# Kernel tuning notes

Measured on AMD Instinct MI355X. Metric: run time of the kernel, lower is better.

## Reference

```python
import jax, jax.numpy as jnp
import numpy as np

N = 4096        # num_queries == gnn_query_dim
C1 = 1001       # classes + 1
D = 4096        # gnn_query_dim
H_MLP = 1024    # mlp_hidden_dim
H = 256         # hidden_dim
O = 256         # output_dim
TOP_K = 32
BN_EPS = 1e-5


def setup_inputs() -> dict:
    key = jax.random.key(0)
    ks = jax.random.split(key, 14)
    def lin(kw, fan_in, shape):
        s = 1.0 / np.sqrt(fan_in)
        return jax.random.uniform(kw, shape, jnp.float32, -s, s)
    return {
        "probs": jax.random.uniform(ks[0], (N, C1), jnp.float32),
        "bbox_coords": jax.random.uniform(ks[1], (N, 4), jnp.float32),
        "query_emb": jax.random.normal(ks[2], (N, D), jnp.float32) * 0.02,
        "node_emb": jax.random.normal(ks[3], (N, D), jnp.float32) * 0.02,
        "mlp_w1": lin(ks[4], D + 4 + C1, (D + 4 + C1, H_MLP)),
        "mlp_b1": lin(ks[5], D + 4 + C1, (H_MLP,)),
        "mlp_w2": lin(ks[6], H_MLP, (H_MLP, N)),
        "mlp_b2": lin(ks[7], H_MLP, (N,)),
        "conv_w1": lin(ks[8], D, (D, H)),
        "conv_b1": lin(ks[9], D, (H,)),
        "conv_w2": lin(ks[10], H, (H, O)),
        "conv_b2": lin(ks[11], H, (O,)),
        "bn_gamma": jnp.ones((H,), jnp.float32),
        "bn_beta": jnp.zeros((H,), jnp.float32),
    }


def reference(probs, bbox_coords, query_emb, node_emb,
              mlp_w1, mlp_b1, mlp_w2, mlp_b2,
              conv_w1, conv_b1, conv_w2, conv_b2,
              bn_gamma, bn_beta):
    # edge-weight MLP -> dense dynamic adjacency logits (N, N)
    ew_in = jnp.concatenate([query_emb, probs, bbox_coords], axis=-1)
    h = jax.nn.relu(ew_in @ mlp_w1 + mlp_b1)
    adj = h @ mlp_w2 + mlp_b2                      # (N, N)

    # top-k neighbors per node (sparse dynamic graph)
    vals, idx = jax.lax.top_k(adj, TOP_K)          # (N, K), (N, K)

    # GCN symmetric normalization from row-degree (sum of top-k weights)
    deg = jnp.sum(vals, axis=-1)                   # (N,)
    dinv = jnp.where(deg > 0, jax.lax.rsqrt(jnp.maximum(deg, 1e-12)), 0.0)
    wn = vals * dinv[:, None] * dinv[idx]          # (N, K)

    def gcn_conv(x, w, b):
        # gather neighbor features, weighted sum, then linear
        msg = jnp.einsum('nk,nkf->nf', wn, x[idx])  # (N, F)
        return msg @ w + b

    out = gcn_conv(node_emb, conv_w1, conv_b1)      # (N, H)
    # BatchNorm1d (batch statistics, training-mode math)
    mean = jnp.mean(out, axis=0)
    var = jnp.var(out, axis=0)
    out = (out - mean) * jax.lax.rsqrt(var + BN_EPS) * bn_gamma + bn_beta
    out = jax.nn.relu(out)
    # dropout is identity in eval mode
    out = gcn_conv(out, conv_w2, conv_b2)           # (N, O)
    return out
```

## Files before the change

### kernel.cpp

```cpp
#include <hip/hip_runtime.h>
#include <cfloat>

#define N_NODES 4096
#define C1_DIM  1001
#define D_DIM   4096
#define HMLP    1024
#define KCAT    (D_DIM + C1_DIM + 4)
#define K1PAD   5120
#define TOPK    32

typedef unsigned short u16;
typedef __bf16 bf16x8 __attribute__((ext_vector_type(8)));
typedef u16    u16x8  __attribute__((ext_vector_type(8)));
typedef float  f32x4  __attribute__((ext_vector_type(4)));

__device__ __forceinline__ u16 f2bf(float f) {
  unsigned u = __float_as_uint(f);
  u += 0x7FFFu + ((u >> 16) & 1u);
  return (u16)(u >> 16);
}
__device__ __forceinline__ float bf2f(u16 h) {
  return __uint_as_float(((unsigned)h) << 16);
}

__device__ __forceinline__ void gload16(const void* g, void* l) {
  __builtin_amdgcn_global_load_lds(
      (const __attribute__((address_space(1))) unsigned int*)g,
      (__attribute__((address_space(3))) unsigned int*)l, 16, 0, 0);
}

__global__ __launch_bounds__(256) void transpose_split(
    const float* __restrict__ in, int R, int C, int Rpad,
    u16* __restrict__ out_hi, u16* __restrict__ out_lo) {
  __shared__ float t[64][65];
  const int rb = blockIdx.x * 64;
  const int cb = blockIdx.y * 64;
  const int tid = threadIdx.x;
  const int lr = tid >> 6, lc = tid & 63;
#pragma unroll
  for (int i = 0; i < 16; ++i) {
    const int r = lr + i * 4;
    const int gr = rb + r;
    t[r][lc] = (gr < R) ? in[(size_t)gr * C + cb + lc] : 0.f;
  }
  __syncthreads();
#pragma unroll
  for (int i = 0; i < 16; ++i) {
    const int c = lr + i * 4;
    const float v = t[lc][c];
    const u16 hi = f2bf(v);
    const u16 lo = f2bf(v - bf2f(hi));
    const size_t o = (size_t)(cb + c) * Rpad + rb + lc;
    out_hi[o] = hi; out_lo[o] = lo;
  }
}

template<int AMODE, bool RELU, bool OUT_SPLIT, bool HASBIAS>
__device__ __forceinline__ void gemm_body(
    int bx, int by,
    const u16* __restrict__ Ahi, const u16* __restrict__ Alo,
    const float* __restrict__ Aq,
    const float* __restrict__ probs, const float* __restrict__ bbox,
    const u16* __restrict__ Bthi, const u16* __restrict__ Btlo,
    const float* __restrict__ bias,
    float* __restrict__ Cf, u16* __restrict__ Chi, u16* __restrict__ Clo,
    int N, int K, u16* lds) {
  const int tid = threadIdx.x;
  const int lane = tid & 63, wave = tid >> 6;
  const int row0 = by * 128, col0 = bx * 64;
  const int wr0 = (wave >> 1) * 64, wc0 = (wave & 1) * 32;
  const int srow = tid >> 2, skof = (tid & 3) * 8;
  const int wu = (tid & ~63) * 8;

  f32x4 acc[4][2];
#pragma unroll
  for (int mi = 0; mi < 4; ++mi)
#pragma unroll
    for (int ni = 0; ni < 2; ++ni) acc[mi][ni] = (f32x4){0.f, 0.f, 0.f, 0.f};

  auto stageB = [&](int buf, int k0) {
    u16* base = lds + buf * 12288;
    gload16(Bthi + (size_t)(col0 + srow) * K + k0 + skof, base + 8192 + wu);
    gload16(Btlo + (size_t)(col0 + srow) * K + k0 + skof, base + 10240 + wu);
  };
  auto stageA0 = [&](int buf, int k0) {
    u16* base = lds + buf * 12288;
    gload16(Ahi + (size_t)(row0 + srow) * K + k0 + skof,      base + wu);
    gload16(Ahi + (size_t)(row0 + 64 + srow) * K + k0 + skof, base + 2048 + wu);
    gload16(Alo + (size_t)(row0 + srow) * K + k0 + skof,      base + 4096 + wu);
    gload16(Alo + (size_t)(row0 + 64 + srow) * K + k0 + skof, base + 6144 + wu);
  };
  auto loadA1 = [&](int k0, float4* x) {
    const int kk = k0 + skof;
#pragma unroll
    for (int j = 0; j < 2; ++j) {
      const int grow = row0 + srow + j * 64;
      if (kk < D_DIM) {
        const float* src = Aq + (size_t)grow * D_DIM + kk;
        x[j * 2]     = *(const float4*)src;
        x[j * 2 + 1] = *(const float4*)(src + 4);
      } else {
        float v[8];
#pragma unroll
        for (int e = 0; e < 8; ++e) {
          const int c = kk + e - D_DIM;
          v[e] = (c < C1_DIM) ? probs[(size_t)grow * C1_DIM + c]
               : (c < C1_DIM + 4) ? bbox[(size_t)grow * 4 + (c - C1_DIM)] : 0.f;
        }
        x[j * 2]     = make_float4(v[0], v[1], v[2], v[3]);
        x[j * 2 + 1] = make_float4(v[4], v[5], v[6], v[7]);
      }
    }
  };
  auto writeA1 = [&](int buf, const float4* x) {
    u16* base = lds + buf * 12288;
#pragma unroll
    for (int j = 0; j < 2; ++j) {
      const float xs[8] = {x[j*2].x, x[j*2].y, x[j*2].z, x[j*2].w,
                           x[j*2+1].x, x[j*2+1].y, x[j*2+1].z, x[j*2+1].w};
      u16x8 hi, lo;
#pragma unroll
      for (int e = 0; e < 8; ++e) {
        const u16 hh = f2bf(xs[e]);
        hi[e] = hh;
        lo[e] = f2bf(xs[e] - bf2f(hh));
      }
      *(u16x8*)&base[(srow + j * 64) * 32 + skof] = hi;
      *(u16x8*)&base[4096 + (srow + j * 64) * 32 + skof] = lo;
    }
  };
  auto compute = [&](int buf) {
    u16* base = lds + buf * 12288;
    const int ko = (lane >> 4) * 8;
    const int ar = lane & 15;
    bf16x8 ah[4], al[4], bh[2], bl[2];
#pragma unroll
    for (int mi = 0; mi < 4; ++mi) {
      const int r = wr0 + mi * 16 + ar;
      ah[mi] = *(const bf16x8*)&base[r * 32 + ko];
      al[mi] = *(const bf16x8*)&base[4096 + r * 32 + ko];
    }
#pragma unroll
    for (int ni = 0; ni < 2; ++ni) {
      const int c = wc0 + ni * 16 + ar;
      bh[ni] = *(const bf16x8*)&base[8192 + c * 32 + ko];
      bl[ni] = *(const bf16x8*)&base[10240 + c * 32 + ko];
    }
#pragma unroll
    for (int mi = 0; mi < 4; ++mi)
#pragma unroll
      for (int ni = 0; ni < 2; ++ni) {
        acc[mi][ni] = __builtin_amdgcn_mfma_f32_16x16x32_bf16(ah[mi], bh[ni], acc[mi][ni], 0, 0, 0);
        acc[mi][ni] = __builtin_amdgcn_mfma_f32_16x16x32_bf16(ah[mi], bl[ni], acc[mi][ni], 0, 0, 0);
        acc[mi][ni] = __builtin_amdgcn_mfma_f32_16x16x32_bf16(al[mi], bh[ni], acc[mi][ni], 0, 0, 0);
      }
  };

  int cur = 0;
  if (AMODE == 0) {
    stageA0(0, 0); stageB(0, 0);
    __syncthreads();
    for (int k0 = 0; k0 < K; k0 += 32) {
      if (k0 + 32 < K) { stageA0(cur ^ 1, k0 + 32); stageB(cur ^ 1, k0 + 32); }
      compute(cur);
      __syncthreads();
      cur ^= 1;
    }
  } else {
    float4 x[4];
    loadA1(0, x); stageB(0, 0); writeA1(0, x);
    __syncthreads();
    for (int k0 = 0; k0 < K; k0 += 32) {
      const bool nx = (k0 + 32 < K);
      float4 xn[4];
      if (nx) { loadA1(k0 + 32, xn); stageB(cur ^ 1, k0 + 32); }
      compute(cur);
      if (nx) writeA1(cur ^ 1, xn);
      __syncthreads();
      cur ^= 1;
    }
  }

#pragma unroll
  for (int mi = 0; mi < 4; ++mi)
#pragma unroll
    for (int ni = 0; ni < 2; ++ni) {
      const int gcol = col0 + wc0 + ni * 16 + (lane & 15);
      const float b = HASBIAS ? bias[gcol] : 0.f;
#pragma unroll
      for (int r = 0; r < 4; ++r) {
        const int grow = row0 + wr0 + mi * 16 + (lane >> 4) * 4 + r;
        float v = acc[mi][ni][r] + b;
        if (RELU) v = fmaxf(v, 0.f);
        if (OUT_SPLIT) {
          const u16 hi = f2bf(v);
          Chi[(size_t)grow * N + gcol] = hi;
          Clo[(size_t)grow * N + gcol] = f2bf(v - bf2f(hi));
        } else {
          Cf[(size_t)grow * N + gcol] = v;
        }
      }
    }
}

__global__ __launch_bounds__(256, 2) void gemm1_kernel(
    const float* __restrict__ query, const float* __restrict__ probs,
    const float* __restrict__ bbox,
    const u16* __restrict__ w1t_hi, const u16* __restrict__ w1t_lo,
    const float* __restrict__ b1,
    u16* __restrict__ h_hi, u16* __restrict__ h_lo) {
  __shared__ u16 lds[2 * 12288];
  gemm_body<1, true, true, true>(blockIdx.x, blockIdx.y,
      nullptr, nullptr, query, probs, bbox, w1t_hi, w1t_lo, b1,
      nullptr, h_hi, h_lo, HMLP, K1PAD, lds);
}

__global__ __launch_bounds__(256, 2) void fused2_kernel(
    const u16* __restrict__ h_hi, const u16* __restrict__ h_lo,
    const u16* __restrict__ w2t_hi, const u16* __restrict__ w2t_lo,
    const float* __restrict__ b2, float* __restrict__ adj,
    const float* __restrict__ node,
    const u16* __restrict__ w1ct_hi, const u16* __restrict__ w1ct_lo,
    float* __restrict__ Z1) {
  __shared__ u16 lds[2 * 12288];
  const int bid = blockIdx.x;
  if (bid < 128) {
    gemm_body<1, false, false, false>(bid & 3, bid >> 2,
        nullptr, nullptr, node, nullptr, nullptr, w1ct_hi, w1ct_lo, nullptr,
        Z1, nullptr, nullptr, 256, D_DIM, lds);
  } else {
    const int r = bid - 128;
    gemm_body<0, false, false, true>(r & 63, r >> 6,
        h_hi, h_lo, nullptr, nullptr, nullptr, w2t_hi, w2t_lo, b2,
        adj, nullptr, nullptr, N_NODES, HMLP, lds);
  }
}

__global__ __launch_bounds__(256) void gemm_small(
    const float* __restrict__ A, const float* __restrict__ B,
    float* __restrict__ C, int M, int Ncols, int K) {
  __shared__ float As[16][68];
  __shared__ float Bs[16][68];
  const int tid = threadIdx.x;
  const int row0 = blockIdx.y * 64, col0 = blockIdx.x * 64;
  const int tx = tid & 15, ty = tid >> 4;
  const int arow = tid >> 2, acol = (tid & 3) * 4;
  const int brow = tid >> 4, bcol = (tid & 15) * 4;

  float acc[4][4];
#pragma unroll
  for (int i = 0; i < 4; ++i)
#pragma unroll
    for (int j = 0; j < 4; ++j) acc[i][j] = 0.f;

  for (int k0 = 0; k0 < K; k0 += 16) {
    const float4 a4 = *(const float4*)(A + (size_t)(row0 + arow) * K + k0 + acol);
    const float4 b4 = *(const float4*)(B + (size_t)(k0 + brow) * Ncols + col0 + bcol);
    __syncthreads();
    As[acol + 0][arow] = a4.x; As[acol + 1][arow] = a4.y;
    As[acol + 2][arow] = a4.z; As[acol + 3][arow] = a4.w;
    *(float4*)&Bs[brow][bcol] = b4;
    __syncthreads();
#pragma unroll
    for (int k = 0; k < 16; ++k) {
      float av[4], bw[4];
      *(float4*)&av[0] = *(const float4*)&As[k][ty * 4];
      *(float4*)&bw[0] = *(const float4*)&Bs[k][tx * 4];
#pragma unroll
      for (int i = 0; i < 4; ++i)
#pragma unroll
        for (int j = 0; j < 4; ++j) acc[i][j] += av[i] * bw[j];
    }
  }

#pragma unroll
  for (int i = 0; i < 4; ++i) {
    const int r = row0 + ty * 4 + i;
    float4 v;
    v.x = acc[i][0]; v.y = acc[i][1]; v.z = acc[i][2]; v.w = acc[i][3];
    *(float4*)(C + (size_t)r * Ncols + col0 + tx * 4) = v;
  }
}

__global__ __launch_bounds__(256) void topk_kernel(
    const float* __restrict__ adj, float* __restrict__ vals,
    int* __restrict__ idxo, float* __restrict__ dinv) {
  __shared__ float sv[N_NODES];
  __shared__ float rw[4];
  __shared__ int   iw[4];
  const int n = blockIdx.x, tid = threadIdx.x;
  const int lane = tid & 63, wave = tid >> 6;
  const float4* rowp = (const float4*)(adj + (size_t)n * N_NODES);

  float mv = -FLT_MAX; int mi = 0x7FFFFFFF;
  for (int g = tid; g < N_NODES / 4; g += 256) {
    const float4 v4 = rowp[g];
    *(float4*)&sv[g * 4] = v4;
    if (v4.x > mv) { mv = v4.x; mi = g * 4 + 0; }
    if (v4.y > mv) { mv = v4.y; mi = g * 4 + 1; }
    if (v4.z > mv) { mv = v4.z; mi = g * 4 + 2; }
    if (v4.w > mv) { mv = v4.w; mi = g * 4 + 3; }
  }

  float sum = 0.f;
  for (int it = 0; it < TOPK; ++it) {
    float bv = mv; int bi = mi;
#pragma unroll
    for (int off = 1; off < 64; off <<= 1) {
      const float ov = __shfl_xor(bv, off);
      const int   oi = __shfl_xor(bi, off);
      if (ov > bv || (ov == bv && oi < bi)) { bv = ov; bi = oi; }
    }
    if (lane == 0) { rw[wave] = bv; iw[wave] = bi; }
    __syncthreads();
    bv = rw[0]; bi = iw[0];
#pragma unroll
    for (int w = 1; w < 4; ++w) {
      const float ov = rw[w]; const int oi = iw[w];
      if (ov > bv || (ov == bv && oi < bi)) { bv = ov; bi = oi; }
    }
    if (tid == 0) {
      vals[(size_t)n * TOPK + it] = bv;
      idxo[(size_t)n * TOPK + it] = bi;
    }
    sum += bv;
    if (tid == ((bi >> 2) & 255)) {
      sv[bi] = -FLT_MAX;
      mv = -FLT_MAX; mi = 0x7FFFFFFF;
      for (int g = tid; g < N_NODES / 4; g += 256) {
#pragma unroll
        for (int e = 0; e < 4; ++e) {
          const float v = sv[g * 4 + e];
          if (v > mv) { mv = v; mi = g * 4 + e; }
        }
      }
    }
    __syncthreads();
  }
  if (tid == 0)
    dinv[n] = (sum > 0.f) ? rsqrtf(fmaxf(sum, 1e-12f)) : 0.f;
}

__global__ __launch_bounds__(256) void agg_kernel(
    const float* __restrict__ Z, const float* __restrict__ vals,
    const int* __restrict__ idxo, const float* __restrict__ dinv,
    const float* __restrict__ bias, float* __restrict__ out) {
  const int n = blockIdx.x, f = threadIdx.x;
  const float dn = dinv[n];
  float acc = bias[f];
#pragma unroll
  for (int k = 0; k < TOPK; ++k) {
    const int   j = idxo[n * TOPK + k];
    const float w = vals[n * TOPK + k] * dn * dinv[j];
    acc += w * Z[(size_t)j * 256 + f];
  }
  out[(size_t)n * 256 + f] = acc;
}

__global__ __launch_bounds__(256) void bn_partial(
    const float* __restrict__ x, float* __restrict__ partial) {
  const int b = blockIdx.x, c = threadIdx.x;
  float s = 0.f, s2 = 0.f;
  for (int r = b * 32; r < b * 32 + 32; ++r) {
    const float v = x[(size_t)r * 256 + c];
    s += v; s2 += v * v;
  }
  partial[(size_t)b * 512 + c]       = s;
  partial[(size_t)b * 512 + 256 + c] = s2;
}

__global__ __launch_bounds__(256) void bn_reduce(
    const float* __restrict__ partial, float* __restrict__ colstats) {
  const int j = blockIdx.x, t = threadIdx.x;
  __shared__ float red[128];
  if (t < 128) red[t] = partial[(size_t)t * 512 + j];
  __syncthreads();
  for (int s = 64; s > 0; s >>= 1) {
    if (t < s) red[t] += red[t + s];
    __syncthreads();
  }
  if (t == 0) colstats[j] = red[0];
}

__global__ __launch_bounds__(256) void bn_apply(
    float* __restrict__ x, const float* __restrict__ colstats,
    const float* __restrict__ gamma, const float* __restrict__ beta) {
  const int i = blockIdx.x * 256 + threadIdx.x;
  const int c = i & 255;
  const float mean = colstats[c] * (1.f / 4096.f);
  float var = colstats[256 + c] * (1.f / 4096.f) - mean * mean;
  var = fmaxf(var, 0.f);
  const float v = (x[i] - mean) * rsqrtf(var + 1e-5f) * gamma[c] + beta[c];
  x[i] = fmaxf(v, 0.f);
}

extern "C" void kernel_launch(void* const* d_in, const int* in_sizes, int n_in,
                              void* d_out, int out_size, void* d_ws, size_t ws_size,
                              hipStream_t stream) {
  const float* probs   = (const float*)d_in[0];
  const float* bbox    = (const float*)d_in[1];
  const float* query   = (const float*)d_in[2];
  const float* node    = (const float*)d_in[3];
  const float* mlp_w1  = (const float*)d_in[4];
  const float* mlp_b1  = (const float*)d_in[5];
  const float* mlp_w2  = (const float*)d_in[6];
  const float* mlp_b2  = (const float*)d_in[7];
  const float* conv_w1 = (const float*)d_in[8];
  const float* conv_b1 = (const float*)d_in[9];
  const float* conv_w2 = (const float*)d_in[10];
  const float* conv_b2 = (const float*)d_in[11];
  const float* gamma   = (const float*)d_in[12];
  const float* beta    = (const float*)d_in[13];

  float* ws = (float*)d_ws;
  size_t off = 0;
  float* adj  = ws + off;  off += (size_t)N_NODES * N_NODES;
  u16* w1t_hi = (u16*)(ws + off);
  u16* w1t_lo = w1t_hi + (size_t)HMLP * K1PAD;
  off += (size_t)HMLP * K1PAD;
  u16* h_hi = (u16*)(ws + off);
  u16* h_lo = h_hi + (size_t)N_NODES * HMLP;
  off += (size_t)N_NODES * HMLP;
  u16* w1ct_hi = (u16*)(ws + off);
  u16* w1ct_lo = w1ct_hi + (size_t)256 * D_DIM;
  const size_t w1ct_off = off;
  off += (size_t)256 * D_DIM;
  float* vals = ws + off;  off += (size_t)N_NODES * TOPK;
  int*   idxo = (int*)(ws + off); off += (size_t)N_NODES * TOPK;
  float* dinv = ws + off;  off += N_NODES;
  float* Z1   = ws + off;  off += (size_t)N_NODES * 256;
  u16* w2t_hi = w1t_hi;
  u16* w2t_lo = w2t_hi + (size_t)N_NODES * HMLP;
  float* out1 = ws + w1ct_off;
  float* Z2       = adj;
  float* partial  = adj + (size_t)N_NODES * 256;
  float* colstats = partial + 128 * 512;

  transpose_split<<<dim3(K1PAD / 64, HMLP / 64), 256, 0, stream>>>(
      mlp_w1, KCAT, HMLP, K1PAD, w1t_hi, w1t_lo);
  transpose_split<<<dim3(D_DIM / 64, 256 / 64), 256, 0, stream>>>(
      conv_w1, D_DIM, 256, D_DIM, w1ct_hi, w1ct_lo);
  gemm1_kernel<<<dim3(HMLP / 64, N_NODES / 128), 256, 0, stream>>>(
      query, probs, bbox, w1t_hi, w1t_lo, mlp_b1, h_hi, h_lo);
  transpose_split<<<dim3(HMLP / 64, N_NODES / 64), 256, 0, stream>>>(
      mlp_w2, HMLP, N_NODES, HMLP, w2t_hi, w2t_lo);
  fused2_kernel<<<128 + (N_NODES / 64) * (N_NODES / 128), 256, 0, stream>>>(
      h_hi, h_lo, w2t_hi, w2t_lo, mlp_b2, adj, node, w1ct_hi, w1ct_lo, Z1);
  topk_kernel<<<N_NODES, 256, 0, stream>>>(adj, vals, idxo, dinv);
  agg_kernel<<<N_NODES, 256, 0, stream>>>(Z1, vals, idxo, dinv, conv_b1, out1);
  bn_partial<<<128, 256, 0, stream>>>(out1, partial);
  bn_reduce<<<512, 256, 0, stream>>>(partial, colstats);
  bn_apply<<<N_NODES, 256, 0, stream>>>(out1, colstats, gamma, beta);
  gemm_small<<<dim3(256 / 64, N_NODES / 64), 256, 0, stream>>>(
      out1, conv_w2, Z2, N_NODES, 256, 256);
  agg_kernel<<<N_NODES, 256, 0, stream>>>(Z2, vals, idxo, dinv, conv_b2, (float*)d_out);
}
```

Before: 642.7 us.

## Prebuild padded probs/bbox tail, pack bf16 splits, swizzle tiles, raise occupancy

Adds a small kernel that copies probs and bbox into a zero-padded 1024-wide float buffer, so the GEMM1 A-loader can always use aligned float4 loads and skip scalar gathers with bounds checks. The bf16 hi/lo split now packs pairs into 32-bit words and writes them to LDS as uint4. The fused second kernel remaps adj tile indices so neighbouring blocks share operand tiles in cache. Launch bounds go from 2 to 3 blocks per SM, which may cause register spills. The cost is an extra launch and an extra 16 MB write-and-read pass through the adj buffer.

```diff
diff --git a/kernel.cpp b/kernel.cpp
--- a/kernel.cpp
+++ b/kernel.cpp
@@ -11,22 +11,28 @@
 
 typedef unsigned short u16;
 typedef __bf16 bf16x8 __attribute__((ext_vector_type(8)));
-typedef u16    u16x8  __attribute__((ext_vector_type(8)));
 typedef float  f32x4  __attribute__((ext_vector_type(4)));
 
-__device__ __forceinline__ u16 f2bf(float f) {
-  unsigned u = __float_as_uint(f);
-  u += 0x7FFFu + ((u >> 16) & 1u);
-  return (u16)(u >> 16);
-}
-__device__ __forceinline__ float bf2f(u16 h) {
-  return __uint_as_float(((unsigned)h) << 16);
+__device__ __forceinline__ unsigned rne_bits(float x) {
+  const unsigned u = __float_as_uint(x);
+  return u + 0x7FFFu + ((u >> 16) & 1u);
 }
 
 __device__ __forceinline__ void gload16(const void* g, void* l) {
   __builtin_amdgcn_global_load_lds(
       (const __attribute__((address_space(1))) unsigned int*)g,
       (__attribute__((address_space(3))) unsigned int*)l, 16, 0, 0);
+}
+
+__global__ __launch_bounds__(256) void tail_build(
+    const float* __restrict__ probs, const float* __restrict__ bbox,
+    float* __restrict__ tail) {
+  const int i = blockIdx.x * 256 + threadIdx.x;
+  const int n = i >> 10, c = i & 1023;
+  float v = 0.f;
+  if (c < C1_DIM)          v = probs[n * C1_DIM + c];
+  else if (c < C1_DIM + 4) v = bbox[n * 4 + (c - C1_DIM)];
+  tail[i] = v;
 }
 
 __global__ __launch_bounds__(256) void transpose_split(
@@ -48,10 +54,11 @@
   for (int i = 0; i < 16; ++i) {
     const int c = lr + i * 4;
     const float v = t[lc][c];
-    const u16 hi = f2bf(v);
-    const u16 lo = f2bf(v - bf2f(hi));
+    const unsigned vh = rne_bits(v);
+    const float r = v - __uint_as_float(vh & 0xFFFF0000u);
     const size_t o = (size_t)(cb + c) * Rpad + rb + lc;
-    out_hi[o] = hi; out_lo[o] = lo;
+    out_hi[o] = (u16)(vh >> 16);
+    out_lo[o] = (u16)(rne_bits(r) >> 16);
   }
 }
 
@@ -59,8 +66,7 @@
 __device__ __forceinline__ void gemm_body(
     int bx, int by,
     const u16* __restrict__ Ahi, const u16* __restrict__ Alo,
-    const float* __restrict__ Aq,
-    const float* __restrict__ probs, const float* __restrict__ bbox,
+    const float* __restrict__ Aq, const float* __restrict__ Atail,
     const u16* __restrict__ Bthi, const u16* __restrict__ Btlo,
     const float* __restrict__ bias,
     float* __restrict__ Cf, u16* __restrict__ Chi, u16* __restrict__ Clo,
@@ -95,21 +101,11 @@
 #pragma unroll
     for (int j = 0; j < 2; ++j) {
       const int grow = row0 + srow + j * 64;
-      if (kk < D_DIM) {
-        const float* src = Aq + (size_t)grow * D_DIM + kk;
-        x[j * 2]     = *(const float4*)src;
-        x[j * 2 + 1] = *(const float4*)(src + 4);
-      } else {
-        float v[8];
-#pragma unroll
-        for (int e = 0; e < 8; ++e) {
-          const int c = kk + e - D_DIM;
-          v[e] = (c < C1_DIM) ? probs[(size_t)grow * C1_DIM + c]
-               : (c < C1_DIM + 4) ? bbox[(size_t)grow * 4 + (c - C1_DIM)] : 0.f;
-        }
-        x[j * 2]     = make_float4(v[0], v[1], v[2], v[3]);
-        x[j * 2 + 1] = make_float4(v[4], v[5], v[6], v[7]);
-      }
+      const float* src = (kk < D_DIM)
+          ? Aq    + (size_t)grow * D_DIM + kk
+          : Atail + (size_t)grow * 1024 + (kk - D_DIM);
+      x[j * 2]     = *(const float4*)src;
+      x[j * 2 + 1] = *(const float4*)(src + 4);
     }
   };
   auto writeA1 = [&](int buf, const float4* x) {
@@ -118,15 +114,18 @@
     for (int j = 0; j < 2; ++j) {
       const float xs[8] = {x[j*2].x, x[j*2].y, x[j*2].z, x[j*2].w,
                            x[j*2+1].x, x[j*2+1].y, x[j*2+1].z, x[j*2+1].w};
-      u16x8 hi, lo;
-#pragma unroll
-      for (int e = 0; e < 8; ++e) {
-        const u16 hh = f2bf(xs[e]);
-        hi[e] = hh;
-        lo[e] = f2bf(xs[e] - bf2f(hh));
+      unsigned hw[4], lw[4];
+#pragma unroll
+      for (int p = 0; p < 4; ++p) {
+        const unsigned v0 = rne_bits(xs[2*p]);
+        const unsigned v1 = rne_bits(xs[2*p+1]);
+        hw[p] = (v1 & 0xFFFF0000u) | (v0 >> 16);
+        const float r0 = xs[2*p]   - __uint_as_float(v0 & 0xFFFF0000u);
+        const float r1 = xs[2*p+1] - __uint_as_float(v1 & 0xFFFF0000u);
+        lw[p] = (rne_bits(r1) & 0xFFFF0000u) | (rne_bits(r0) >> 16);
       }
-      *(u16x8*)&base[(srow + j * 64) * 32 + skof] = hi;
-      *(u16x8*)&base[4096 + (srow + j * 64) * 32 + skof] = lo;
+      *(uint4*)&base[(srow + j * 64) * 32 + skof] = make_uint4(hw[0], hw[1], hw[2], hw[3]);
+      *(uint4*)&base[4096 + (srow + j * 64) * 32 + skof] = make_uint4(lw[0], lw[1], lw[2], lw[3]);
     }
   };
   auto compute = [&](int buf) {
@@ -193,9 +192,10 @@
         float v = acc[mi][ni][r] + b;
         if (RELU) v = fmaxf(v, 0.f);
         if (OUT_SPLIT) {
-          const u16 hi = f2bf(v);
-          Chi[(size_t)grow * N + gcol] = hi;
-          Clo[(size_t)grow * N + gcol] = f2bf(v - bf2f(hi));
+          const unsigned vh = rne_bits(v);
+          Chi[(size_t)grow * N + gcol] = (u16)(vh >> 16);
+          const float rr = v - __uint_as_float(vh & 0xFFFF0000u);
+          Clo[(size_t)grow * N + gcol] = (u16)(rne_bits(rr) >> 16);
         } else {
           Cf[(size_t)grow * N + gcol] = v;
         }
@@ -203,19 +203,18 @@
     }
 }
 
-__global__ __launch_bounds__(256, 2) void gemm1_kernel(
-    const float* __restrict__ query, const float* __restrict__ probs,
-    const float* __restrict__ bbox,
+__global__ __launch_bounds__(256, 3) void gemm1_kernel(
+    const float* __restrict__ query, const float* __restrict__ tail,
     const u16* __restrict__ w1t_hi, const u16* __restrict__ w1t_lo,
     const float* __restrict__ b1,
     u16* __restrict__ h_hi, u16* __restrict__ h_lo) {
   __shared__ u16 lds[2 * 12288];
   gemm_body<1, true, true, true>(blockIdx.x, blockIdx.y,
-      nullptr, nullptr, query, probs, bbox, w1t_hi, w1t_lo, b1,
+      nullptr, nullptr, query, tail, w1t_hi, w1t_lo, b1,
       nullptr, h_hi, h_lo, HMLP, K1PAD, lds);
 }
 
-__global__ __launch_bounds__(256, 2) void fused2_kernel(
+__global__ __launch_bounds__(256, 3) void fused2_kernel(
     const u16* __restrict__ h_hi, const u16* __restrict__ h_lo,
     const u16* __restrict__ w2t_hi, const u16* __restrict__ w2t_lo,
     const float* __restrict__ b2, float* __restrict__ adj,
@@ -226,12 +225,13 @@
   const int bid = blockIdx.x;
   if (bid < 128) {
     gemm_body<1, false, false, false>(bid & 3, bid >> 2,
-        nullptr, nullptr, node, nullptr, nullptr, w1ct_hi, w1ct_lo, nullptr,
+        nullptr, nullptr, node, nullptr, w1ct_hi, w1ct_lo, nullptr,
         Z1, nullptr, nullptr, 256, D_DIM, lds);
   } else {
     const int r = bid - 128;
-    gemm_body<0, false, false, true>(r & 63, r >> 6,
-        h_hi, h_lo, nullptr, nullptr, nullptr, w2t_hi, w2t_lo, b2,
+    const int swz = (r & 7) * 256 + (r >> 3);
+    gemm_body<0, false, false, true>(swz & 63, swz >> 6,
+        h_hi, h_lo, nullptr, nullptr, w2t_hi, w2t_lo, b2,
         adj, nullptr, nullptr, N_NODES, HMLP, lds);
   }
 }
@@ -429,6 +429,7 @@
   int*   idxo = (int*)(ws + off); off += (size_t)N_NODES * TOPK;
   float* dinv = ws + off;  off += N_NODES;
   float* Z1   = ws + off;  off += (size_t)N_NODES * 256;
+  float* tail = adj;
   u16* w2t_hi = w1t_hi;
   u16* w2t_lo = w2t_hi + (size_t)N_NODES * HMLP;
   float* out1 = ws + w1ct_off;
@@ -436,12 +437,13 @@
   float* partial  = adj + (size_t)N_NODES * 256;
   float* colstats = partial + 128 * 512;
 
+  tail_build<<<(N_NODES * 1024) / 256, 256, 0, stream>>>(probs, bbox, tail);
   transpose_split<<<dim3(K1PAD / 64, HMLP / 64), 256, 0, stream>>>(
       mlp_w1, KCAT, HMLP, K1PAD, w1t_hi, w1t_lo);
   transpose_split<<<dim3(D_DIM / 64, 256 / 64), 256, 0, stream>>>(
       conv_w1, D_DIM, 256, D_DIM, w1ct_hi, w1ct_lo);
   gemm1_kernel<<<dim3(HMLP / 64, N_NODES / 128), 256, 0, stream>>>(
-      query, probs, bbox, w1t_hi, w1t_lo, mlp_b1, h_hi, h_lo);
+      query, tail, w1t_hi, w1t_lo, mlp_b1, h_hi, h_lo);
   transpose_split<<<dim3(HMLP / 64, N_NODES / 64), 256, 0, stream>>>(
       mlp_w2, HMLP, N_NODES, HMLP, w2t_hi, w2t_lo);
   fused2_kernel<<<128 + (N_NODES / 64) * (N_NODES / 128), 256, 0, stream>>>(
```

Result: slower. 714.0 us (+11.1%).
